# Kernel tuning notes

Hardware: AMD Instinct MI355X
Metric: run time of the kernel (lower is better)

Reference implementation:

```python
import jax, jax.numpy as jnp
import numpy as np
import math

B, S, D, H = 2, 2048, 1024, 16
DK = D // H


def setup_inputs() -> dict:
    key = jax.random.key(0)
    ks = jax.random.split(key, 12)
    scale = 1.0 / math.sqrt(D)
    inp = {
        "query": jax.random.normal(ks[0], (B, S, D), jnp.float32),
        "key": jax.random.normal(ks[1], (B, S, D), jnp.float32),
        "value": jax.random.normal(ks[2], (B, S, D), jnp.float32),
        # causal 0/1 mask, broadcast over heads
        "mask": jnp.broadcast_to(jnp.tril(jnp.ones((S, S), jnp.int32)), (B, 1, S, S)),
        "Wq": jax.random.normal(ks[3], (D, D), jnp.float32) * scale,
        "bq": jnp.zeros((D,), jnp.float32),
        "Wk": jax.random.normal(ks[4], (D, D), jnp.float32) * scale,
        "bk": jnp.zeros((D,), jnp.float32),
        "Wv": jax.random.normal(ks[5], (D, D), jnp.float32) * scale,
        "bv": jnp.zeros((D,), jnp.float32),
        "Wo": jax.random.normal(ks[6], (D, D), jnp.float32) * scale,
        "bo": jnp.zeros((D,), jnp.float32),
    }
    return inp


def _split_heads(x):
    # [B,S,D] -> [B,H,S,DK]
    return x.reshape(B, S, H, DK).transpose(0, 2, 1, 3)


def reference(query, key, value, mask, Wq, bq, Wk, bk, Wv, bv, Wo, bo):
    q = _split_heads(query @ Wq.T + bq)
    k = _split_heads(key @ Wk.T + bk)
    v = _split_heads(value @ Wv.T + bv)
    # scaled dot-product attention with additive mask (mask==0 -> -inf)
    scores = jnp.einsum("bhqd,bhkd->bhqk", q, k) / math.sqrt(DK)
    scores = jnp.where(mask == 0, -jnp.inf, scores)
    w = jax.nn.softmax(scores, axis=-1)
    out = jnp.einsum("bhqk,bhkd->bhqd", w, v)
    out = out.transpose(0, 2, 1, 3).reshape(B, S, D)
    return out @ Wo.T + bo
```

## Files before the change

### kernel.cpp

```cpp
#include <hip/hip_runtime.h>
#include <hip/hip_bf16.h>
#include <math.h>

#define BBATCH 2
#define SSEQ 2048
#define DMODEL 1024
#define NH 16
#define MTOT (BBATCH*SSEQ)

typedef short bfrag __attribute__((ext_vector_type(8)));
typedef float ffrag __attribute__((ext_vector_type(4)));

typedef const __attribute__((address_space(1))) unsigned int* gas_t;
typedef __attribute__((address_space(3))) unsigned int* las_t;

__device__ __forceinline__ void dl16(const void* g, void* l) {
  __builtin_amdgcn_global_load_lds((gas_t)(unsigned long long)g,
                                   (las_t)(unsigned int)(unsigned long long)l,
                                   16, 0, 0);
}

__device__ __forceinline__ void drain_vm() {
  asm volatile("s_waitcnt vmcnt(0)" ::: "memory");
}

#if defined(__has_builtin) && __has_builtin(__builtin_amdgcn_exp2f)
__device__ __forceinline__ float fexp2(float x) { return __builtin_amdgcn_exp2f(x); }
#else
__device__ __forceinline__ float fexp2(float x) { return exp2f(x); }
#endif

__device__ __forceinline__ unsigned short f2bf(float f) {
  union { float f; unsigned u; } v; v.f = f;
  unsigned r = v.u + 0x7fffu + ((v.u >> 16) & 1u);
  return (unsigned short)(r >> 16);
}

__global__ __launch_bounds__(256) void convert_all_kernel(
    const float* __restrict__ q, const float* __restrict__ k, const float* __restrict__ v,
    const float* __restrict__ wq, const float* __restrict__ wk,
    const float* __restrict__ wv, const float* __restrict__ wo,
    unsigned short* __restrict__ dst)
{
  const long NIN = (long)MTOT * DMODEL;
  const long NW  = (long)DMODEL * DMODEL;
  const long total8 = (3 * NIN + 4 * NW) >> 3;
  long i8 = (long)blockIdx.x * blockDim.x + threadIdx.x;
  const long stride = (long)gridDim.x * blockDim.x;
  for (; i8 < total8; i8 += stride) {
    const long i = i8 << 3;
    const float* src; long off;
    if (i < NIN)          { src = q; off = i; }
    else if (i < 2 * NIN) { src = k; off = i - NIN; }
    else if (i < 3 * NIN) { src = v; off = i - 2 * NIN; }
    else {
      const long j = i - 3 * NIN;
      const int wsel = (int)(j >> 20);
      off = j & (NW - 1);
      src = (wsel == 0) ? wq : (wsel == 1) ? wk : (wsel == 2) ? wv : wo;
    }
    const float4 x0 = *(const float4*)(src + off);
    const float4 x1 = *(const float4*)(src + off + 4);
    ushort4 o0, o1;
    o0.x = f2bf(x0.x); o0.y = f2bf(x0.y); o0.z = f2bf(x0.z); o0.w = f2bf(x0.w);
    o1.x = f2bf(x1.x); o1.y = f2bf(x1.y); o1.z = f2bf(x1.z); o1.w = f2bf(x1.w);
    union { ushort4 s[2]; uint4 u; } pk; pk.s[0] = o0; pk.s[1] = o1;
    *(uint4*)(dst + i) = pk.u;
  }
}

struct ProjArgs {
  const unsigned short* X[3];
  const unsigned short* W[3];
  const float* bias[3];
  unsigned short* dst[3];
  float scale[3];
};

__global__ __launch_bounds__(256, 2) void qkv_proj(ProjArgs a)
{
  __shared__ alignas(16) unsigned short As[2][128 * 64];
  __shared__ alignas(16) unsigned short Bs[2][128 * 64];
  const int t = threadIdx.x;
  const int lane = t & 63, w = t >> 6;
  const int quad = lane >> 4, l16 = lane & 15;
  const int m0 = blockIdx.x * 128;
  const int n0 = blockIdx.y * 128;
  const int z = blockIdx.z;
  const unsigned short* __restrict__ X = a.X[z];
  const unsigned short* __restrict__ W = a.W[z];
  const int wm = (w & 1) * 64, wn = (w >> 1) * 64;

  int sw[2];
#pragma unroll
  for (int c = 0; c < 2; ++c) sw[c] = (((c * 4 + quad) ^ (l16 & 7)) * 8);

  ffrag acc[4][4];
#pragma unroll
  for (int i = 0; i < 4; ++i)
#pragma unroll
    for (int j = 0; j < 4; ++j)
#pragma unroll
      for (int e = 0; e < 4; ++e) acc[i][j][e] = 0.f;

#pragma unroll
  for (int i = 0; i < 4; ++i) {
    const int ch = i * 256 + t;
    const int row = ch >> 3, lc = (ch & 7) ^ (row & 7);
    dl16(X + (size_t)(m0 + row) * DMODEL + lc * 8, As[0] + ch * 8);
    dl16(W + (size_t)(n0 + row) * DMODEL + lc * 8, Bs[0] + ch * 8);
  }

  for (int kk = 0; kk < 16; ++kk) {
    const int cur = kk & 1;
    drain_vm();
    __syncthreads();

    if (kk < 15) {
      const int k1 = (kk + 1) * 64, nxt = cur ^ 1;
#pragma unroll
      for (int i = 0; i < 4; ++i) {
        const int ch = i * 256 + t;
        const int row = ch >> 3, lc = (ch & 7) ^ (row & 7);
        dl16(X + (size_t)(m0 + row) * DMODEL + k1 + lc * 8, As[nxt] + ch * 8);
        dl16(W + (size_t)(n0 + row) * DMODEL + k1 + lc * 8, Bs[nxt] + ch * 8);
      }
    }

    bfrag af[4][2], bg[4][2];
#pragma unroll
    for (int fi = 0; fi < 4; ++fi)
#pragma unroll
      for (int c = 0; c < 2; ++c) {
        af[fi][c] = *(const bfrag*)&As[cur][(wm + fi * 16 + l16) * 64 + sw[c]];
        bg[fi][c] = *(const bfrag*)&Bs[cur][(wn + fi * 16 + l16) * 64 + sw[c]];
      }
#pragma unroll
    for (int c = 0; c < 2; ++c)
#pragma unroll
      for (int fi = 0; fi < 4; ++fi)
#pragma unroll
        for (int fj = 0; fj < 4; ++fj)
          acc[fi][fj] = __builtin_amdgcn_mfma_f32_16x16x32_bf16(af[fi][c], bg[fj][c], acc[fi][fj], 0, 0, 0);
  }

  const float sc = a.scale[z];
  const float* __restrict__ bias = a.bias[z];
  unsigned short* __restrict__ dst = a.dst[z];
#pragma unroll
  for (int fj = 0; fj < 4; ++fj) {
    const int n = n0 + wn + fj * 16 + l16;
    const float bv = bias[n];
    const int h = n >> 6, dk = n & 63;
    if (z < 2) {
#pragma unroll
      for (int fi = 0; fi < 4; ++fi)
#pragma unroll
        for (int r = 0; r < 4; ++r) {
          const int m = m0 + wm + fi * 16 + quad * 4 + r;
          const int b_ = m >> 11, s_ = m & (SSEQ - 1);
          dst[((size_t)(b_ * NH + h) * SSEQ + s_) * 64 + dk] = f2bf((acc[fi][fj][r] + bv) * sc);
        }
    } else {
#pragma unroll
      for (int fi = 0; fi < 4; ++fi) {
        const int m = m0 + wm + fi * 16 + quad * 4;
        const int b_ = m >> 11, s_ = m & (SSEQ - 1);
        ushort4 pk;
        pk.x = f2bf(acc[fi][fj][0] + bv);
        pk.y = f2bf(acc[fi][fj][1] + bv);
        pk.z = f2bf(acc[fi][fj][2] + bv);
        pk.w = f2bf(acc[fi][fj][3] + bv);
        *(ushort4*)&dst[((size_t)(b_ * NH + h) * 64 + dk) * SSEQ + s_] = pk;
      }
    }
  }
}

__global__ __launch_bounds__(256, 2) void out_proj(
    const unsigned short* __restrict__ X,
    const unsigned short* __restrict__ W,
    const float* __restrict__ bias,
    float* __restrict__ Y)
{
  __shared__ alignas(16) unsigned short As[2][128 * 64];
  __shared__ alignas(16) unsigned short Bs[2][64 * 64];
  const int t = threadIdx.x;
  const int lane = t & 63, w = t >> 6;
  const int quad = lane >> 4, l16 = lane & 15;
  const int m0 = blockIdx.x * 128;
  const int n0 = blockIdx.y * 64;
  const int wm = (w & 1) * 64, wn = (w >> 1) * 32;

  int sw[2];
#pragma unroll
  for (int c = 0; c < 2; ++c) sw[c] = (((c * 4 + quad) ^ (l16 & 7)) * 8);

  ffrag acc[4][2];
#pragma unroll
  for (int i = 0; i < 4; ++i)
#pragma unroll
    for (int j = 0; j < 2; ++j)
#pragma unroll
      for (int e = 0; e < 4; ++e) acc[i][j][e] = 0.f;

#pragma unroll
  for (int i = 0; i < 4; ++i) {
    const int ch = i * 256 + t;
    const int row = ch >> 3, lc = (ch & 7) ^ (row & 7);
    dl16(X + (size_t)(m0 + row) * DMODEL + lc * 8, As[0] + ch * 8);
  }
#pragma unroll
  for (int i = 0; i < 2; ++i) {
    const int ch = i * 256 + t;
    const int row = ch >> 3, lc = (ch & 7) ^ (row & 7);
    dl16(W + (size_t)(n0 + row) * DMODEL + lc * 8, Bs[0] + ch * 8);
  }

  for (int kk = 0; kk < 16; ++kk) {
    const int cur = kk & 1;
    drain_vm();
    __syncthreads();

    if (kk < 15) {
      const int k1 = (kk + 1) * 64, nxt = cur ^ 1;
#pragma unroll
      for (int i = 0; i < 4; ++i) {
        const int ch = i * 256 + t;
        const int row = ch >> 3, lc = (ch & 7) ^ (row & 7);
        dl16(X + (size_t)(m0 + row) * DMODEL + k1 + lc * 8, As[nxt] + ch * 8);
      }
#pragma unroll
      for (int i = 0; i < 2; ++i) {
        const int ch = i * 256 + t;
        const int row = ch >> 3, lc = (ch & 7) ^ (row & 7);
        dl16(W + (size_t)(n0 + row) * DMODEL + k1 + lc * 8, Bs[nxt] + ch * 8);
      }
    }

    bfrag af[4][2], bg[2][2];
#pragma unroll
    for (int fi = 0; fi < 4; ++fi)
#pragma unroll
      for (int c = 0; c < 2; ++c)
        af[fi][c] = *(const bfrag*)&As[cur][(wm + fi * 16 + l16) * 64 + sw[c]];
#pragma unroll
    for (int fj = 0; fj < 2; ++fj)
#pragma unroll
      for (int c = 0; c < 2; ++c)
        bg[fj][c] = *(const bfrag*)&Bs[cur][(wn + fj * 16 + l16) * 64 + sw[c]];
#pragma unroll
    for (int c = 0; c < 2; ++c)
#pragma unroll
      for (int fi = 0; fi < 4; ++fi)
#pragma unroll
        for (int fj = 0; fj < 2; ++fj)
          acc[fi][fj] = __builtin_amdgcn_mfma_f32_16x16x32_bf16(af[fi][c], bg[fj][c], acc[fi][fj], 0, 0, 0);
  }

#pragma unroll
  for (int fj = 0; fj < 2; ++fj) {
    const int n = n0 + wn + fj * 16 + l16;
    const float bv = bias[n];
#pragma unroll
    for (int fi = 0; fi < 4; ++fi)
#pragma unroll
      for (int r = 0; r < 4; ++r) {
        const int m = m0 + wm + fi * 16 + quad * 4 + r;
        Y[(size_t)m * DMODEL + n] = acc[fi][fj][r] + bv;
      }
  }
}

__global__ __launch_bounds__(256, 4) void attn_mfma(
    const unsigned short* __restrict__ Q,
    const unsigned short* __restrict__ K,
    const unsigned short* __restrict__ Vt_g,
    unsigned short* __restrict__ ctx)
{
  __shared__ alignas(16) unsigned short Kb[2][64 * 64];
  __shared__ alignas(16) unsigned short Vb[2][64 * 64];
  __shared__ alignas(16) unsigned short Pt[4][16 * 64];

  const int t = threadIdx.x;
  const int lane = t & 63, w = t >> 6;
  const int quad = lane >> 4, l16 = lane & 15;
  const int bh = blockIdx.y;
  const int qtile = blockIdx.z ? (31 - (int)blockIdx.x) : (int)blockIdx.x;
  const int i0 = qtile * 64;
  const int b_ = bh >> 4, h_ = bh & (NH - 1);
  const int q_l = w * 16 + l16;

  const unsigned short* kg = K + (size_t)bh * SSEQ * 64;
  const unsigned short* vg = Vt_g + (size_t)bh * 64 * SSEQ;

  int koff[2], voff[2], loff[2];
#pragma unroll
  for (int i = 0; i < 2; ++i) {
    const int ch = i * 256 + t;
    const int r = ch >> 3;
    const int lc = (ch & 7) ^ (r & 7);
    koff[i] = r * 64 + lc * 8;
    voff[i] = r * SSEQ + lc * 8;
    loff[i] = ch * 8;
  }
  int sw[2];
#pragma unroll
  for (int c = 0; c < 2; ++c) sw[c] = (((c * 4 + quad) ^ (l16 & 7)) * 8);
  const int pwr = l16 * 64 + (quad & 1) * 4;

#pragma unroll
  for (int i = 0; i < 2; ++i) {
    dl16(kg + koff[i], Kb[0] + loff[i]);
    dl16(vg + voff[i], Vb[0] + loff[i]);
  }

  const unsigned short* qg = Q + ((size_t)bh * SSEQ + i0) * 64;
  bfrag qb[2];
#pragma unroll
  for (int c = 0; c < 2; ++c)
    qb[c] = *(const bfrag*)(qg + (size_t)q_l * 64 + c * 32 + quad * 8);

  bfrag onesf;
#pragma unroll
  for (int j = 0; j < 8; ++j) onesf[j] = (short)0x3F80;

  ffrag o[4], lacc;
#pragma unroll
  for (int fn = 0; fn < 4; ++fn)
#pragma unroll
    for (int e = 0; e < 4; ++e) o[fn][e] = 0.f;
#pragma unroll
  for (int e = 0; e < 4; ++e) lacc[e] = 0.f;

  for (int jt = 0; jt < qtile + 1; ++jt) {
    const int cur = jt & 1;
    const bool diag = (jt == qtile);
    drain_vm();
    __syncthreads();

    if (!diag) {
      const int nxt = cur ^ 1;
#pragma unroll
      for (int i = 0; i < 2; ++i) {
        dl16(kg + (size_t)(jt + 1) * 4096 + koff[i], Kb[nxt] + loff[i]);
        dl16(vg + (size_t)(jt + 1) * 64   + voff[i], Vb[nxt] + loff[i]);
      }
    }

    ffrag s[4];
#pragma unroll
    for (int fj = 0; fj < 4; ++fj)
#pragma unroll
      for (int e = 0; e < 4; ++e) s[fj][e] = 0.f;
#pragma unroll
    for (int c = 0; c < 2; ++c)
#pragma unroll
      for (int fj = 0; fj < 4; ++fj) {
        bfrag ka = *(const bfrag*)&Kb[cur][(fj * 16 + l16) * 64 + sw[c]];
        s[fj] = __builtin_amdgcn_mfma_f32_16x16x32_bf16(ka, qb[c], s[fj], 0, 0, 0);
      }

    if (diag) {
#pragma unroll
      for (int fj = 0; fj < 4; ++fj) {
        float p[4];
#pragma unroll
        for (int r = 0; r < 4; ++r) {
          const float pe = fexp2(s[fj][r]);
          p[r] = ((fj * 16 + quad * 4 + r) > q_l) ? 0.f : pe;
        }
        float2 lo; lo.x = p[0]; lo.y = p[1];
        float2 hi; hi.x = p[2]; hi.y = p[3];
        union { __hip_bfloat162 h[2]; unsigned long long u; } cv;
        cv.h[0] = __float22bfloat162_rn(lo);
        cv.h[1] = __float22bfloat162_rn(hi);
        const int cc = fj * 2 + (quad >> 1);
        *(unsigned long long*)&Pt[w][pwr + ((cc ^ (l16 & 7)) * 8)] = cv.u;
      }
    } else {
#pragma unroll
      for (int fj = 0; fj < 4; ++fj) {
        float2 lo; lo.x = fexp2(s[fj][0]); lo.y = fexp2(s[fj][1]);
        float2 hi; hi.x = fexp2(s[fj][2]); hi.y = fexp2(s[fj][3]);
        union { __hip_bfloat162 h[2]; unsigned long long u; } cv;
        cv.h[0] = __float22bfloat162_rn(lo);
        cv.h[1] = __float22bfloat162_rn(hi);
        const int cc = fj * 2 + (quad >> 1);
        *(unsigned long long*)&Pt[w][pwr + ((cc ^ (l16 & 7)) * 8)] = cv.u;
      }
    }
    asm volatile("s_waitcnt lgkmcnt(0)" ::: "memory");

#pragma unroll
    for (int c = 0; c < 2; ++c) {
      bfrag pb = *(const bfrag*)&Pt[w][l16 * 64 + sw[c]];
      lacc = __builtin_amdgcn_mfma_f32_16x16x32_bf16(onesf, pb, lacc, 0, 0, 0);
#pragma unroll
      for (int fn = 0; fn < 4; ++fn) {
        bfrag va = *(const bfrag*)&Vb[cur][(fn * 16 + l16) * 64 + sw[c]];
        o[fn] = __builtin_amdgcn_mfma_f32_16x16x32_bf16(va, pb, o[fn], 0, 0, 0);
      }
    }
  }

  const float inv = 1.f / lacc[0];
  unsigned short* cbase = ctx + (size_t)(b_ * SSEQ + i0 + q_l) * DMODEL + h_ * 64;
#pragma unroll
  for (int fn = 0; fn < 4; ++fn) {
    float2 lo; lo.x = o[fn][0] * inv; lo.y = o[fn][1] * inv;
    float2 hi; hi.x = o[fn][2] * inv; hi.y = o[fn][3] * inv;
    union { __hip_bfloat162 h[2]; unsigned long long u; } cv;
    cv.h[0] = __float22bfloat162_rn(lo);
    cv.h[1] = __float22bfloat162_rn(hi);
    *(unsigned long long*)(cbase + fn * 16 + quad * 4) = cv.u;
  }
}

extern "C" void kernel_launch(void* const* d_in, const int* in_sizes, int n_in,
                              void* d_out, int out_size, void* d_ws, size_t ws_size,
                              hipStream_t stream)
{
  const float* q  = (const float*)d_in[0];
  const float* k  = (const float*)d_in[1];
  const float* v  = (const float*)d_in[2];
  const float* wq = (const float*)d_in[4];
  const float* bq = (const float*)d_in[5];
  const float* wk = (const float*)d_in[6];
  const float* bk = (const float*)d_in[7];
  const float* wv = (const float*)d_in[8];
  const float* bv = (const float*)d_in[9];
  const float* wo = (const float*)d_in[10];
  const float* bo = (const float*)d_in[11];

  const long NIN = (long)MTOT * DMODEL;
  const long NW  = (long)DMODEL * DMODEL;
  unsigned short* ws16 = (unsigned short*)d_ws;
  unsigned short* qx  = ws16;
  unsigned short* kx  = qx + NIN;
  unsigned short* vx  = kx + NIN;
  unsigned short* wqb = vx + NIN;
  unsigned short* wkb = wqb + NW;
  unsigned short* wvb = wkb + NW;
  unsigned short* wob = wvb + NW;
  unsigned short* Qp  = wob + NW;
  unsigned short* Kp  = Qp + NIN;
  unsigned short* Vp  = Kp + NIN;
  unsigned short* Cx  = Vp + NIN;

  convert_all_kernel<<<2048, 256, 0, stream>>>(q, k, v, wq, wk, wv, wo, ws16);

  ProjArgs pa;
  pa.X[0] = qx;  pa.X[1] = kx;  pa.X[2] = vx;
  pa.W[0] = wqb; pa.W[1] = wkb; pa.W[2] = wvb;
  pa.bias[0] = bq; pa.bias[1] = bk; pa.bias[2] = bv;
  pa.dst[0] = Qp; pa.dst[1] = Kp; pa.dst[2] = Vp;
  pa.scale[0] = 0.18033688011112042f;
  pa.scale[1] = 1.0f;
  pa.scale[2] = 1.0f;
  qkv_proj<<<dim3(MTOT / 128, DMODEL / 128, 3), 256, 0, stream>>>(pa);

  attn_mfma<<<dim3(16, BBATCH * NH, 2), 256, 0, stream>>>(Qp, Kp, Vp, Cx);

  out_proj<<<dim3(MTOT / 128, DMODEL / 64), 256, 0, stream>>>(Cx, wob, bo, (float*)d_out);
}
```

Baseline: 228.3 us.

## Pair low and high causal query tiles per block to share K/V tiles

Each attention block now handles two query tiles, x and 31-x, so that causal work is balanced across blocks and every loaded K/V tile serves both query tiles while their ranges overlap. This halves the grid and the number of K/V loads from global memory for the shared prefix. It doubles the per-thread accumulators and P scratch and lowers the launch-bounds occupancy hint from 4 to 2, so fewer blocks may hide latency, and only 512 blocks remain to fill the GPU.

```diff
diff --git a/kernel.cpp b/kernel.cpp
--- a/kernel.cpp
+++ b/kernel.cpp
@@ -272,7 +272,42 @@
   }
 }
 
-__global__ __launch_bounds__(256, 4) void attn_mfma(
+__device__ __forceinline__ void softmax_pack(
+    const ffrag* s, const bool diag, const int q_l, const int quad,
+    const int l16, const int pwr, unsigned short* pt)
+{
+  if (diag) {
+#pragma unroll
+    for (int fj = 0; fj < 4; ++fj) {
+      float p[4];
+#pragma unroll
+      for (int r = 0; r < 4; ++r) {
+        const float pe = fexp2(s[fj][r]);
+        p[r] = ((fj * 16 + quad * 4 + r) > q_l) ? 0.f : pe;
+      }
+      float2 lo; lo.x = p[0]; lo.y = p[1];
+      float2 hi; hi.x = p[2]; hi.y = p[3];
+      union { __hip_bfloat162 h[2]; unsigned long long u; } cv;
+      cv.h[0] = __float22bfloat162_rn(lo);
+      cv.h[1] = __float22bfloat162_rn(hi);
+      const int cc = fj * 2 + (quad >> 1);
+      *(unsigned long long*)&pt[pwr + ((cc ^ (l16 & 7)) * 8)] = cv.u;
+    }
+  } else {
+#pragma unroll
+    for (int fj = 0; fj < 4; ++fj) {
+      float2 lo; lo.x = fexp2(s[fj][0]); lo.y = fexp2(s[fj][1]);
+      float2 hi; hi.x = fexp2(s[fj][2]); hi.y = fexp2(s[fj][3]);
+      union { __hip_bfloat162 h[2]; unsigned long long u; } cv;
+      cv.h[0] = __float22bfloat162_rn(lo);
+      cv.h[1] = __float22bfloat162_rn(hi);
+      const int cc = fj * 2 + (quad >> 1);
+      *(unsigned long long*)&pt[pwr + ((cc ^ (l16 & 7)) * 8)] = cv.u;
+    }
+  }
+}
+
+__global__ __launch_bounds__(256, 2) void attn_mfma(
     const unsigned short* __restrict__ Q,
     const unsigned short* __restrict__ K,
     const unsigned short* __restrict__ Vt_g,
@@ -280,14 +315,15 @@
 {
   __shared__ alignas(16) unsigned short Kb[2][64 * 64];
   __shared__ alignas(16) unsigned short Vb[2][64 * 64];
-  __shared__ alignas(16) unsigned short Pt[4][16 * 64];
+  __shared__ alignas(16) unsigned short Pt[4][2][16 * 64];
 
   const int t = threadIdx.x;
   const int lane = t & 63, w = t >> 6;
   const int quad = lane >> 4, l16 = lane & 15;
   const int bh = blockIdx.y;
-  const int qtile = blockIdx.z ? (31 - (int)blockIdx.x) : (int)blockIdx.x;
-  const int i0 = qtile * 64;
+  const int x = blockIdx.x;
+  const int qt_lo = x, qt_hi = 31 - x;
+  const int i0_lo = qt_lo * 64, i0_hi = qt_hi * 64;
   const int b_ = bh >> 4, h_ = bh & (NH - 1);
   const int q_l = w * 16 + l16;
 
@@ -315,31 +351,32 @@
     dl16(vg + voff[i], Vb[0] + loff[i]);
   }
 
-  const unsigned short* qg = Q + ((size_t)bh * SSEQ + i0) * 64;
-  bfrag qb[2];
-#pragma unroll
-  for (int c = 0; c < 2; ++c)
-    qb[c] = *(const bfrag*)(qg + (size_t)q_l * 64 + c * 32 + quad * 8);
+  const unsigned short* qg = Q + (size_t)bh * SSEQ * 64;
+  bfrag qb_lo[2], qb_hi[2];
+#pragma unroll
+  for (int c = 0; c < 2; ++c) {
+    qb_lo[c] = *(const bfrag*)(qg + (size_t)(i0_lo + q_l) * 64 + c * 32 + quad * 8);
+    qb_hi[c] = *(const bfrag*)(qg + (size_t)(i0_hi + q_l) * 64 + c * 32 + quad * 8);
+  }
 
   bfrag onesf;
 #pragma unroll
   for (int j = 0; j < 8; ++j) onesf[j] = (short)0x3F80;
 
-  ffrag o[4], lacc;
+  ffrag o_lo[4], o_hi[4], lac_lo, lac_hi;
 #pragma unroll
   for (int fn = 0; fn < 4; ++fn)
 #pragma unroll
-    for (int e = 0; e < 4; ++e) o[fn][e] = 0.f;
-#pragma unroll
-  for (int e = 0; e < 4; ++e) lacc[e] = 0.f;
-
-  for (int jt = 0; jt < qtile + 1; ++jt) {
+    for (int e = 0; e < 4; ++e) { o_lo[fn][e] = 0.f; o_hi[fn][e] = 0.f; }
+#pragma unroll
+  for (int e = 0; e < 4; ++e) { lac_lo[e] = 0.f; lac_hi[e] = 0.f; }
+
+  for (int jt = 0; jt <= qt_hi; ++jt) {
     const int cur = jt & 1;
-    const bool diag = (jt == qtile);
     drain_vm();
     __syncthreads();
 
-    if (!diag) {
+    if (jt < qt_hi) {
       const int nxt = cur ^ 1;
 #pragma unroll
       for (int i = 0; i < 2; ++i) {
@@ -348,72 +385,86 @@
       }
     }
 
-    ffrag s[4];
-#pragma unroll
-    for (int fj = 0; fj < 4; ++fj)
-#pragma unroll
-      for (int e = 0; e < 4; ++e) s[fj][e] = 0.f;
-#pragma unroll
-    for (int c = 0; c < 2; ++c)
-#pragma unroll
-      for (int fj = 0; fj < 4; ++fj) {
-        bfrag ka = *(const bfrag*)&Kb[cur][(fj * 16 + l16) * 64 + sw[c]];
-        s[fj] = __builtin_amdgcn_mfma_f32_16x16x32_bf16(ka, qb[c], s[fj], 0, 0, 0);
-      }
-
-    if (diag) {
-#pragma unroll
-      for (int fj = 0; fj < 4; ++fj) {
-        float p[4];
-#pragma unroll
-        for (int r = 0; r < 4; ++r) {
-          const float pe = fexp2(s[fj][r]);
-          p[r] = ((fj * 16 + quad * 4 + r) > q_l) ? 0.f : pe;
+    if (jt <= qt_lo) {
+      ffrag s_hi[4], s_lo[4];
+#pragma unroll
+      for (int fj = 0; fj < 4; ++fj)
+#pragma unroll
+        for (int e = 0; e < 4; ++e) { s_hi[fj][e] = 0.f; s_lo[fj][e] = 0.f; }
+#pragma unroll
+      for (int c = 0; c < 2; ++c)
+#pragma unroll
+        for (int fj = 0; fj < 4; ++fj) {
+          bfrag ka = *(const bfrag*)&Kb[cur][(fj * 16 + l16) * 64 + sw[c]];
+          s_hi[fj] = __builtin_amdgcn_mfma_f32_16x16x32_bf16(ka, qb_hi[c], s_hi[fj], 0, 0, 0);
+          s_lo[fj] = __builtin_amdgcn_mfma_f32_16x16x32_bf16(ka, qb_lo[c], s_lo[fj], 0, 0, 0);
         }
-        float2 lo; lo.x = p[0]; lo.y = p[1];
-        float2 hi; hi.x = p[2]; hi.y = p[3];
-        union { __hip_bfloat162 h[2]; unsigned long long u; } cv;
-        cv.h[0] = __float22bfloat162_rn(lo);
-        cv.h[1] = __float22bfloat162_rn(hi);
-        const int cc = fj * 2 + (quad >> 1);
-        *(unsigned long long*)&Pt[w][pwr + ((cc ^ (l16 & 7)) * 8)] = cv.u;
+
+      softmax_pack(s_hi, false, q_l, quad, l16, pwr, &Pt[w][0][0]);
+      softmax_pack(s_lo, jt == qt_lo, q_l, quad, l16, pwr, &Pt[w][1][0]);
+      asm volatile("s_waitcnt lgkmcnt(0)" ::: "memory");
+
+#pragma unroll
+      for (int c = 0; c < 2; ++c) {
+        bfrag pbh = *(const bfrag*)&Pt[w][0][l16 * 64 + sw[c]];
+        bfrag pbl = *(const bfrag*)&Pt[w][1][l16 * 64 + sw[c]];
+        lac_hi = __builtin_amdgcn_mfma_f32_16x16x32_bf16(onesf, pbh, lac_hi, 0, 0, 0);
+        lac_lo = __builtin_amdgcn_mfma_f32_16x16x32_bf16(onesf, pbl, lac_lo, 0, 0, 0);
+#pragma unroll
+        for (int fn = 0; fn < 4; ++fn) {
+          bfrag va = *(const bfrag*)&Vb[cur][(fn * 16 + l16) * 64 + sw[c]];
+          o_hi[fn] = __builtin_amdgcn_mfma_f32_16x16x32_bf16(va, pbh, o_hi[fn], 0, 0, 0);
+          o_lo[fn] = __builtin_amdgcn_mfma_f32_16x16x32_bf16(va, pbl, o_lo[fn], 0, 0, 0);
+        }
       }
     } else {
-#pragma unroll
-      for (int fj = 0; fj < 4; ++fj) {
-        float2 lo; lo.x = fexp2(s[fj][0]); lo.y = fexp2(s[fj][1]);
-        float2 hi; hi.x = fexp2(s[fj][2]); hi.y = fexp2(s[fj][3]);
-        union { __hip_bfloat162 h[2]; unsigned long long u; } cv;
-        cv.h[0] = __float22bfloat162_rn(lo);
-        cv.h[1] = __float22bfloat162_rn(hi);
-        const int cc = fj * 2 + (quad >> 1);
-        *(unsigned long long*)&Pt[w][pwr + ((cc ^ (l16 & 7)) * 8)] = cv.u;
-      }
-    }
-    asm volatile("s_waitcnt lgkmcnt(0)" ::: "memory");
-
-#pragma unroll
-    for (int c = 0; c < 2; ++c) {
-      bfrag pb = *(const bfrag*)&Pt[w][l16 * 64 + sw[c]];
-      lacc = __builtin_amdgcn_mfma_f32_16x16x32_bf16(onesf, pb, lacc, 0, 0, 0);
-#pragma unroll
-      for (int fn = 0; fn < 4; ++fn) {
-        bfrag va = *(const bfrag*)&Vb[cur][(fn * 16 + l16) * 64 + sw[c]];
-        o[fn] = __builtin_amdgcn_mfma_f32_16x16x32_bf16(va, pb, o[fn], 0, 0, 0);
-      }
-    }
-  }
-
-  const float inv = 1.f / lacc[0];
-  unsigned short* cbase = ctx + (size_t)(b_ * SSEQ + i0 + q_l) * DMODEL + h_ * 64;
+      ffrag s_hi[4];
+#pragma unroll
+      for (int fj = 0; fj < 4; ++fj)
+#pragma unroll
+        for (int e = 0; e < 4; ++e) s_hi[fj][e] = 0.f;
+#pragma unroll
+      for (int c = 0; c < 2; ++c)
+#pragma unroll
+        for (int fj = 0; fj < 4; ++fj) {
+          bfrag ka = *(const bfrag*)&Kb[cur][(fj * 16 + l16) * 64 + sw[c]];
+          s_hi[fj] = __builtin_amdgcn_mfma_f32_16x16x32_bf16(ka, qb_hi[c], s_hi[fj], 0, 0, 0);
+        }
+
+      softmax_pack(s_hi, jt == qt_hi, q_l, quad, l16, pwr, &Pt[w][0][0]);
+      asm volatile("s_waitcnt lgkmcnt(0)" ::: "memory");
+
+#pragma unroll
+      for (int c = 0; c < 2; ++c) {
+        bfrag pbh = *(const bfrag*)&Pt[w][0][l16 * 64 + sw[c]];
+        lac_hi = __builtin_amdgcn_mfma_f32_16x16x32_bf16(onesf, pbh, lac_hi, 0, 0, 0);
+#pragma unroll
+        for (int fn = 0; fn < 4; ++fn) {
+          bfrag va = *(const bfrag*)&Vb[cur][(fn * 16 + l16) * 64 + sw[c]];
+          o_hi[fn] = __builtin_amdgcn_mfma_f32_16x16x32_bf16(va, pbh, o_hi[fn], 0, 0, 0);
+        }
+      }
+    }
+  }
+
+  const float inv_lo = 1.f / lac_lo[0];
+  const float inv_hi = 1.f / lac_hi[0];
+  unsigned short* cb_lo = ctx + (size_t)(b_ * SSEQ + i0_lo + q_l) * DMODEL + h_ * 64;
+  unsigned short* cb_hi = ctx + (size_t)(b_ * SSEQ + i0_hi + q_l) * DMODEL + h_ * 64;
 #pragma unroll
   for (int fn = 0; fn < 4; ++fn) {
-    float2 lo; lo.x = o[fn][0] * inv; lo.y = o[fn][1] * inv;
-    float2 hi; hi.x = o[fn][2] * inv; hi.y = o[fn][3] * inv;
+    float2 lo; float2 hi;
     union { __hip_bfloat162 h[2]; unsigned long long u; } cv;
+    lo.x = o_lo[fn][0] * inv_lo; lo.y = o_lo[fn][1] * inv_lo;
+    hi.x = o_lo[fn][2] * inv_lo; hi.y = o_lo[fn][3] * inv_lo;
     cv.h[0] = __float22bfloat162_rn(lo);
     cv.h[1] = __float22bfloat162_rn(hi);
-    *(unsigned long long*)(cbase + fn * 16 + quad * 4) = cv.u;
+    *(unsigned long long*)(cb_lo + fn * 16 + quad * 4) = cv.u;
+    lo.x = o_hi[fn][0] * inv_hi; lo.y = o_hi[fn][1] * inv_hi;
+    hi.x = o_hi[fn][2] * inv_hi; hi.y = o_hi[fn][3] * inv_hi;
+    cv.h[0] = __float22bfloat162_rn(lo);
+    cv.h[1] = __float22bfloat162_rn(hi);
+    *(unsigned long long*)(cb_hi + fn * 16 + quad * 4) = cv.u;
   }
 }
 
@@ -460,7 +511,7 @@
   pa.scale[2] = 1.0f;
   qkv_proj<<<dim3(MTOT / 128, DMODEL / 128, 3), 256, 0, stream>>>(pa);
 
-  attn_mfma<<<dim3(16, BBATCH * NH, 2), 256, 0, stream>>>(Qp, Kp, Vp, Cx);
+  attn_mfma<<<dim3(16, BBATCH * NH), 256, 0, stream>>>(Qp, Kp, Vp, Cx);
 
   out_proj<<<dim3(MTOT / 128, DMODEL / 64), 256, 0, stream>>>(Cx, wob, bo, (float*)d_out);
 }
```

Measured after the change: 225.6 us. No clear change (-1.2%).

## Rewrite attention with 32x32 MFMA, register-resident P, and paired causal tiles

Applied to the files above, without the earlier changes.

The attention kernel now uses 32x32x16 MFMA tiles and keeps the probability matrix in registers, rearranged with permlane32 swaps, instead of staging it through LDS. This removes the LDS round trip and the ones-vector MFMA used for row sums. Each block pairs a low and a high causal query tile so that every block shares the same K/V stream, which halves the grid and balances work across blocks. In exchange there is higher register pressure (occupancy hint lowered from 4 to 2 blocks), and the waves assigned to the short tile sit idle during the later iterations.

```diff
diff --git a/kernel.cpp b/kernel.cpp
--- a/kernel.cpp
+++ b/kernel.cpp
@@ -10,6 +10,8 @@
 
 typedef short bfrag __attribute__((ext_vector_type(8)));
 typedef float ffrag __attribute__((ext_vector_type(4)));
+typedef float f16frag __attribute__((ext_vector_type(16)));
+typedef unsigned int uiv2 __attribute__((ext_vector_type(2)));
 
 typedef const __attribute__((address_space(1))) unsigned int* gas_t;
 typedef __attribute__((address_space(3))) unsigned int* las_t;
@@ -30,10 +32,28 @@
 __device__ __forceinline__ float fexp2(float x) { return exp2f(x); }
 #endif
 
+#if defined(__has_builtin) && __has_builtin(__builtin_amdgcn_permlane32_swap)
+__device__ __forceinline__ void pl32swap(unsigned &a, unsigned &b) {
+  uiv2 r = __builtin_amdgcn_permlane32_swap(a, b, false, false);
+  a = r[0]; b = r[1];
+}
+#else
+__device__ __forceinline__ void pl32swap(unsigned &a, unsigned &b) {
+  asm volatile("v_permlane32_swap_b32 %0, %1" : "+v"(a), "+v"(b));
+}
+#endif
+
 __device__ __forceinline__ unsigned short f2bf(float f) {
   union { float f; unsigned u; } v; v.f = f;
   unsigned r = v.u + 0x7fffu + ((v.u >> 16) & 1u);
   return (unsigned short)(r >> 16);
+}
+
+__device__ __forceinline__ unsigned pkbf2(float a, float b) {
+  float2 f; f.x = a; f.y = b;
+  union { __hip_bfloat162 h; unsigned u; } cv;
+  cv.h = __float22bfloat162_rn(f);
+  return cv.u;
 }
 
 __global__ __launch_bounds__(256) void convert_all_kernel(
@@ -272,7 +292,7 @@
   }
 }
 
-__global__ __launch_bounds__(256, 4) void attn_mfma(
+__global__ __launch_bounds__(256, 2) void attn_mfma(
     const unsigned short* __restrict__ Q,
     const unsigned short* __restrict__ K,
     const unsigned short* __restrict__ Vt_g,
@@ -280,16 +300,19 @@
 {
   __shared__ alignas(16) unsigned short Kb[2][64 * 64];
   __shared__ alignas(16) unsigned short Vb[2][64 * 64];
-  __shared__ alignas(16) unsigned short Pt[4][16 * 64];
 
   const int t = threadIdx.x;
   const int lane = t & 63, w = t >> 6;
-  const int quad = lane >> 4, l16 = lane & 15;
+  const int l31 = lane & 31, h = lane >> 5;
   const int bh = blockIdx.y;
-  const int qtile = blockIdx.z ? (31 - (int)blockIdx.x) : (int)blockIdx.x;
-  const int i0 = qtile * 64;
+  const int x = blockIdx.x;
+  const int qt_lo = x, qt_hi = 31 - x;
+  const int qsel = w >> 1;
+  const int qt_w = qsel ? qt_hi : qt_lo;
+  const int i0_w = qt_w * 64;
+  const int q0 = (w & 1) * 32;
+  const int qloc = q0 + l31;
   const int b_ = bh >> 4, h_ = bh & (NH - 1);
-  const int q_l = w * 16 + l16;
 
   const unsigned short* kg = K + (size_t)bh * SSEQ * 64;
   const unsigned short* vg = Vt_g + (size_t)bh * 64 * SSEQ;
@@ -304,10 +327,10 @@
     voff[i] = r * SSEQ + lc * 8;
     loff[i] = ch * 8;
   }
-  int sw[2];
-#pragma unroll
-  for (int c = 0; c < 2; ++c) sw[c] = (((c * 4 + quad) ^ (l16 & 7)) * 8);
-  const int pwr = l16 * 64 + (quad & 1) * 4;
+  int pc[4];
+#pragma unroll
+  for (int ks = 0; ks < 4; ++ks) pc[ks] = ((ks * 2 + h) ^ (l31 & 7)) * 8;
+  const int rb0 = l31 * 64, rb1 = (32 + l31) * 64;
 
 #pragma unroll
   for (int i = 0; i < 2; ++i) {
@@ -315,31 +338,23 @@
     dl16(vg + voff[i], Vb[0] + loff[i]);
   }
 
-  const unsigned short* qg = Q + ((size_t)bh * SSEQ + i0) * 64;
-  bfrag qb[2];
-#pragma unroll
-  for (int c = 0; c < 2; ++c)
-    qb[c] = *(const bfrag*)(qg + (size_t)q_l * 64 + c * 32 + quad * 8);
-
-  bfrag onesf;
-#pragma unroll
-  for (int j = 0; j < 8; ++j) onesf[j] = (short)0x3F80;
-
-  ffrag o[4], lacc;
-#pragma unroll
-  for (int fn = 0; fn < 4; ++fn)
-#pragma unroll
-    for (int e = 0; e < 4; ++e) o[fn][e] = 0.f;
-#pragma unroll
-  for (int e = 0; e < 4; ++e) lacc[e] = 0.f;
-
-  for (int jt = 0; jt < qtile + 1; ++jt) {
+  const unsigned short* qrow = Q + ((size_t)bh * SSEQ + i0_w + qloc) * 64;
+  bfrag qb[4];
+#pragma unroll
+  for (int ks = 0; ks < 4; ++ks)
+    qb[ks] = *(const bfrag*)(qrow + ks * 16 + h * 8);
+
+  f16frag o0, o1;
+#pragma unroll
+  for (int e = 0; e < 16; ++e) { o0[e] = 0.f; o1[e] = 0.f; }
+  float lacc = 0.f;
+
+  for (int jt = 0; jt <= qt_hi; ++jt) {
     const int cur = jt & 1;
-    const bool diag = (jt == qtile);
     drain_vm();
     __syncthreads();
 
-    if (!diag) {
+    if (jt < qt_hi) {
       const int nxt = cur ^ 1;
 #pragma unroll
       for (int i = 0; i < 2; ++i) {
@@ -348,72 +363,81 @@
       }
     }
 
-    ffrag s[4];
-#pragma unroll
-    for (int fj = 0; fj < 4; ++fj)
-#pragma unroll
-      for (int e = 0; e < 4; ++e) s[fj][e] = 0.f;
-#pragma unroll
-    for (int c = 0; c < 2; ++c)
-#pragma unroll
-      for (int fj = 0; fj < 4; ++fj) {
-        bfrag ka = *(const bfrag*)&Kb[cur][(fj * 16 + l16) * 64 + sw[c]];
-        s[fj] = __builtin_amdgcn_mfma_f32_16x16x32_bf16(ka, qb[c], s[fj], 0, 0, 0);
-      }
-
-    if (diag) {
-#pragma unroll
-      for (int fj = 0; fj < 4; ++fj) {
-        float p[4];
-#pragma unroll
-        for (int r = 0; r < 4; ++r) {
-          const float pe = fexp2(s[fj][r]);
-          p[r] = ((fj * 16 + quad * 4 + r) > q_l) ? 0.f : pe;
+    if (jt <= qt_w) {
+      f16frag s0, s1;
+#pragma unroll
+      for (int e = 0; e < 16; ++e) { s0[e] = 0.f; s1[e] = 0.f; }
+#pragma unroll
+      for (int ks = 0; ks < 4; ++ks) {
+        bfrag ka0 = *(const bfrag*)&Kb[cur][rb0 + pc[ks]];
+        bfrag ka1 = *(const bfrag*)&Kb[cur][rb1 + pc[ks]];
+        s0 = __builtin_amdgcn_mfma_f32_32x32x16_bf16(ka0, qb[ks], s0, 0, 0, 0);
+        s1 = __builtin_amdgcn_mfma_f32_32x32x16_bf16(ka1, qb[ks], s1, 0, 0, 0);
+      }
+
+      const bool diag = (jt == qt_w);
+      float p0[16], p1[16];
+#pragma unroll
+      for (int r = 0; r < 16; ++r) { p0[r] = fexp2(s0[r]); p1[r] = fexp2(s1[r]); }
+      if (diag) {
+#pragma unroll
+        for (int r = 0; r < 16; ++r) {
+          const int keyl = (r & 3) + 8 * (r >> 2) + 4 * h;
+          if (keyl > qloc)      p0[r] = 0.f;
+          if (keyl + 32 > qloc) p1[r] = 0.f;
         }
-        float2 lo; lo.x = p[0]; lo.y = p[1];
-        float2 hi; hi.x = p[2]; hi.y = p[3];
-        union { __hip_bfloat162 h[2]; unsigned long long u; } cv;
-        cv.h[0] = __float22bfloat162_rn(lo);
-        cv.h[1] = __float22bfloat162_rn(hi);
-        const int cc = fj * 2 + (quad >> 1);
-        *(unsigned long long*)&Pt[w][pwr + ((cc ^ (l16 & 7)) * 8)] = cv.u;
-      }
-    } else {
-#pragma unroll
-      for (int fj = 0; fj < 4; ++fj) {
-        float2 lo; lo.x = fexp2(s[fj][0]); lo.y = fexp2(s[fj][1]);
-        float2 hi; hi.x = fexp2(s[fj][2]); hi.y = fexp2(s[fj][3]);
-        union { __hip_bfloat162 h[2]; unsigned long long u; } cv;
-        cv.h[0] = __float22bfloat162_rn(lo);
-        cv.h[1] = __float22bfloat162_rn(hi);
-        const int cc = fj * 2 + (quad >> 1);
-        *(unsigned long long*)&Pt[w][pwr + ((cc ^ (l16 & 7)) * 8)] = cv.u;
-      }
-    }
-    asm volatile("s_waitcnt lgkmcnt(0)" ::: "memory");
-
-#pragma unroll
-    for (int c = 0; c < 2; ++c) {
-      bfrag pb = *(const bfrag*)&Pt[w][l16 * 64 + sw[c]];
-      lacc = __builtin_amdgcn_mfma_f32_16x16x32_bf16(onesf, pb, lacc, 0, 0, 0);
-#pragma unroll
-      for (int fn = 0; fn < 4; ++fn) {
-        bfrag va = *(const bfrag*)&Vb[cur][(fn * 16 + l16) * 64 + sw[c]];
-        o[fn] = __builtin_amdgcn_mfma_f32_16x16x32_bf16(va, pb, o[fn], 0, 0, 0);
-      }
-    }
-  }
-
-  const float inv = 1.f / lacc[0];
-  unsigned short* cbase = ctx + (size_t)(b_ * SSEQ + i0 + q_l) * DMODEL + h_ * 64;
-#pragma unroll
-  for (int fn = 0; fn < 4; ++fn) {
-    float2 lo; lo.x = o[fn][0] * inv; lo.y = o[fn][1] * inv;
-    float2 hi; hi.x = o[fn][2] * inv; hi.y = o[fn][3] * inv;
-    union { __hip_bfloat162 h[2]; unsigned long long u; } cv;
-    cv.h[0] = __float22bfloat162_rn(lo);
-    cv.h[1] = __float22bfloat162_rn(hi);
-    *(unsigned long long*)(cbase + fn * 16 + quad * 4) = cv.u;
+      }
+      float ss = 0.f;
+#pragma unroll
+      for (int r = 0; r < 16; r += 4)
+        ss += ((p0[r] + p0[r + 1]) + (p0[r + 2] + p0[r + 3])) +
+              ((p1[r] + p1[r + 1]) + (p1[r + 2] + p1[r + 3]));
+      lacc += ss;
+
+      bfrag pb[4];
+#pragma unroll
+      for (int ks = 0; ks < 4; ++ks) {
+        const float* pp = (ks >> 1) ? p1 : p0;
+        const int kb = (ks & 1) * 8;
+        unsigned w0 = pkbf2(pp[kb + 0], pp[kb + 1]);
+        unsigned w1 = pkbf2(pp[kb + 2], pp[kb + 3]);
+        unsigned w2 = pkbf2(pp[kb + 4], pp[kb + 5]);
+        unsigned w3 = pkbf2(pp[kb + 6], pp[kb + 7]);
+        pl32swap(w0, w2);
+        pl32swap(w1, w3);
+        union { unsigned u[4]; bfrag f; } cv;
+        cv.u[0] = w0; cv.u[1] = w1; cv.u[2] = w2; cv.u[3] = w3;
+        pb[ks] = cv.f;
+      }
+
+#pragma unroll
+      for (int ks = 0; ks < 4; ++ks) {
+        bfrag va0 = *(const bfrag*)&Vb[cur][rb0 + pc[ks]];
+        bfrag va1 = *(const bfrag*)&Vb[cur][rb1 + pc[ks]];
+        o0 = __builtin_amdgcn_mfma_f32_32x32x16_bf16(va0, pb[ks], o0, 0, 0, 0);
+        o1 = __builtin_amdgcn_mfma_f32_32x32x16_bf16(va1, pb[ks], o1, 0, 0, 0);
+      }
+    }
+  }
+
+  const float lfull = lacc + __shfl_xor(lacc, 32, 64);
+  const float inv = 1.f / lfull;
+  unsigned short* cb = ctx + (size_t)(b_ * SSEQ + i0_w + qloc) * DMODEL + h_ * 64;
+#pragma unroll
+  for (int g = 0; g < 4; ++g) {
+    const int dkb = 8 * g + 4 * h;
+    union { __hip_bfloat162 hh[2]; unsigned long long u; } cv;
+    float2 lo, hi;
+    lo.x = o0[4 * g + 0] * inv; lo.y = o0[4 * g + 1] * inv;
+    hi.x = o0[4 * g + 2] * inv; hi.y = o0[4 * g + 3] * inv;
+    cv.hh[0] = __float22bfloat162_rn(lo);
+    cv.hh[1] = __float22bfloat162_rn(hi);
+    *(unsigned long long*)(cb + dkb) = cv.u;
+    lo.x = o1[4 * g + 0] * inv; lo.y = o1[4 * g + 1] * inv;
+    hi.x = o1[4 * g + 2] * inv; hi.y = o1[4 * g + 3] * inv;
+    cv.hh[0] = __float22bfloat162_rn(lo);
+    cv.hh[1] = __float22bfloat162_rn(hi);
+    *(unsigned long long*)(cb + 32 + dkb) = cv.u;
   }
 }
 
@@ -460,7 +484,7 @@
   pa.scale[2] = 1.0f;
   qkv_proj<<<dim3(MTOT / 128, DMODEL / 128, 3), 256, 0, stream>>>(pa);
 
-  attn_mfma<<<dim3(16, BBATCH * NH, 2), 256, 0, stream>>>(Qp, Kp, Vp, Cx);
+  attn_mfma<<<dim3(16, BBATCH * NH), 256, 0, stream>>>(Qp, Kp, Vp, Cx);
 
   out_proj<<<dim3(MTOT / 128, DMODEL / 64), 256, 0, stream>>>(Cx, wob, bo, (float*)d_out);
 }
```

Measured after the change: 226.5 us. No clear change (-0.8%).
